# Kernel optimization log

Measured on AMD Instinct MI355X. Metric: run time of the kernel, lower is better.

## Reference

```python
import jax, jax.numpy as jnp
import numpy as np

GRID_D = 1024
SEQ_D = 1024
POS_D = 512
H = 16
HEAD = SEQ_D // H
MULT = 4
EPS = 1e-5


def layer_norm(x, g, b, eps=EPS):
    mu = jnp.mean(x, axis=-1, keepdims=True)
    var = jnp.mean(jnp.square(x - mu), axis=-1, keepdims=True)
    return (x - mu) * jax.lax.rsqrt(var + eps) * g + b


def setup_inputs() -> dict:
    key = jax.random.key(0)
    ks = jax.random.split(key, 12)
    std = 0.02
    B, N, M, L = 16, 16, 16, 1024
    return {
        "grid": jax.random.normal(ks[0], (B, N, M, GRID_D), jnp.float32),
        "query_pos": jax.random.normal(ks[1], (B, L, POS_D), jnp.float32),
        "Wq": jax.random.normal(ks[2], (POS_D, SEQ_D), jnp.float32) * std,
        "Wk": jax.random.normal(ks[3], (GRID_D, SEQ_D), jnp.float32) * std,
        "Wv": jax.random.normal(ks[4], (GRID_D, SEQ_D), jnp.float32) * std,
        "Wo": jax.random.normal(ks[5], (SEQ_D, SEQ_D), jnp.float32) * std,
        "ln_grid_g": jnp.ones((SEQ_D,), jnp.float32),
        "ln_grid_b": jnp.zeros((SEQ_D,), jnp.float32),
        "ln_q_g": jnp.ones((POS_D,), jnp.float32),
        "ln_q_b": jnp.zeros((POS_D,), jnp.float32),
        "ln_mlp_g": jnp.ones((SEQ_D,), jnp.float32),
        "ln_mlp_b": jnp.zeros((SEQ_D,), jnp.float32),
        "W1": jax.random.normal(ks[6], (SEQ_D, MULT * SEQ_D), jnp.float32) * std,
        "b1": jnp.zeros((MULT * SEQ_D,), jnp.float32),
        "W2": jax.random.normal(ks[7], (MULT * SEQ_D, SEQ_D), jnp.float32) * std,
        "b2": jnp.zeros((SEQ_D,), jnp.float32),
    }


def reference(grid, query_pos, Wq, Wk, Wv, Wo,
              ln_grid_g, ln_grid_b, ln_q_g, ln_q_b, ln_mlp_g, ln_mlp_b,
              W1, b1, W2, b2):
    B, N, M, _ = grid.shape
    T = N * M
    grid_flat = grid.reshape(B, T, GRID_D)
    K = layer_norm(jnp.einsum('btd,de->bte', grid_flat, Wk), ln_grid_g, ln_grid_b)
    V = jnp.einsum('btd,de->bte', grid_flat, Wv)
    qn = layer_norm(query_pos, ln_q_g, ln_q_b)
    Q = jnp.einsum('bld,de->ble', qn, Wq)  # (B, L, seq_d)
    L = Q.shape[1]
    # split heads: (B, H, len, head)
    Qh = Q.reshape(B, L, H, HEAD).transpose(0, 2, 1, 3)
    Kh = K.reshape(B, T, H, HEAD).transpose(0, 2, 1, 3)
    Vh = V.reshape(B, T, H, HEAD).transpose(0, 2, 1, 3)
    scale = 1.0 / np.sqrt(HEAD).astype(np.float32)
    scores = jnp.einsum('bhld,bhmd->bhlm', Qh, Kh) * scale
    probs = jax.nn.softmax(scores, axis=-1)
    attn = jnp.einsum('bhlm,bhmd->bhld', probs, Vh)
    attn = attn.transpose(0, 2, 1, 3).reshape(B, L, SEQ_D)
    attn = jnp.einsum('bld,de->ble', attn, Wo)
    x = Q + attn  # Q_proj in the torch code equals Q
    xn = layer_norm(x, ln_mlp_g, ln_mlp_b)
    h = jax.nn.gelu(jnp.einsum('bld,dh->blh', xn, W1) + b1)
    mlp_out = jnp.einsum('blh,hd->bld', h, W2) + b2
    return x + mlp_out
```

## Files before the change

kernel.cpp:

```cpp
#include <hip/hip_runtime.h>
#include <hip/hip_bf16.h>
#include <stdint.h>

typedef unsigned short u16;
typedef __bf16 bf16x8 __attribute__((ext_vector_type(8)));
typedef float f32x4 __attribute__((ext_vector_type(4)));

__device__ __forceinline__ float bf2f(unsigned int u) {
  union { float f; unsigned int i; } v; v.i = u << 16; return v.f;
}
__device__ __forceinline__ u16 f2bf(float f) {
  union { float f; unsigned int i; } v; v.f = f;
  unsigned int r = v.i + 0x7fffu + ((v.i >> 16) & 1u);
  return (u16)(r >> 16);
}

__device__ __forceinline__ float fast_gelu(float u) {
  const float z = -u * (1.5957691216057308f + 0.07135481282121989f * u * u);
  return u * __builtin_amdgcn_rcpf(1.0f + __expf(z));
}

__device__ __forceinline__ void gl_lds16(const void* g, void* l) {
  __builtin_amdgcn_global_load_lds(
      (const __attribute__((address_space(1))) unsigned int*)(uintptr_t)g,
      (__attribute__((address_space(3))) unsigned int*)(uintptr_t)l,
      16, 0, 0);
}

__global__ __launch_bounds__(256) void k_cast_bf16(const float* __restrict__ in,
                                                   u16* __restrict__ out, int n4) {
  int i = blockIdx.x * blockDim.x + threadIdx.x;
  if (i < n4) {
    float4 v = ((const float4*)in)[i];
    ushort4 o;
    o.x = f2bf(v.x); o.y = f2bf(v.y); o.z = f2bf(v.z); o.w = f2bf(v.w);
    ((ushort4*)out)[i] = o;
  }
}

__global__ __launch_bounds__(256) void k_transpose_cast(const float* __restrict__ in,
                                                        u16* __restrict__ out,
                                                        int K, int N) {
  __shared__ float tile[64][65];
  const int k0 = blockIdx.y * 64, n0 = blockIdx.x * 64;
  const int t = threadIdx.x;
#pragma unroll
  for (int i = 0; i < 16; i++) {
    int lin = t + i * 256, kk = lin >> 6, nn = lin & 63;
    tile[kk][nn] = in[(size_t)(k0 + kk) * N + n0 + nn];
  }
  __syncthreads();
#pragma unroll
  for (int i = 0; i < 16; i++) {
    int lin = t + i * 256, nn = lin >> 6, kk = lin & 63;
    out[(size_t)(n0 + nn) * K + k0 + kk] = f2bf(tile[kk][nn]);
  }
}

__global__ __launch_bounds__(256) void k_transpose3(const float* __restrict__ in0,
                                                    const float* __restrict__ in1,
                                                    const float* __restrict__ in2,
                                                    u16* __restrict__ out0,
                                                    u16* __restrict__ out1,
                                                    u16* __restrict__ out2) {
  __shared__ float tile[64][65];
  const float* in = (blockIdx.z == 0) ? in0 : (blockIdx.z == 1) ? in1 : in2;
  u16* out = (blockIdx.z == 0) ? out0 : (blockIdx.z == 1) ? out1 : out2;
  const int k0 = blockIdx.y * 64, n0 = blockIdx.x * 64;
  const int t = threadIdx.x;
#pragma unroll
  for (int i = 0; i < 16; i++) {
    int lin = t + i * 256, kk = lin >> 6, nn = lin & 63;
    tile[kk][nn] = in[(size_t)(k0 + kk) * 1024 + n0 + nn];
  }
  __syncthreads();
#pragma unroll
  for (int i = 0; i < 16; i++) {
    int lin = t + i * 256, nn = lin >> 6, kk = lin & 63;
    out[(size_t)(n0 + nn) * 1024 + k0 + kk] = f2bf(tile[kk][nn]);
  }
}

template <int RL>
__global__ __launch_bounds__(256) void k_ln_f32(const float* __restrict__ in,
                                                u16* __restrict__ out,
                                                const float* __restrict__ g,
                                                const float* __restrict__ b, int nrows) {
  const int wid = threadIdx.x >> 6, lane = threadIdx.x & 63;
  const int row = blockIdx.x * 4 + wid;
  if (row >= nrows) return;
  constexpr int PER = RL / 64;
  constexpr int NC = PER / 4;
  const float* p = in + (size_t)row * RL;
  float v[PER];
#pragma unroll
  for (int i = 0; i < NC; i++) {
    float4 f = ((const float4*)p)[lane + i * 64];
    v[i * 4 + 0] = f.x; v[i * 4 + 1] = f.y; v[i * 4 + 2] = f.z; v[i * 4 + 3] = f.w;
  }
  float s = 0.f, ss = 0.f;
#pragma unroll
  for (int i = 0; i < PER; i++) { s += v[i]; ss += v[i] * v[i]; }
#pragma unroll
  for (int o = 32; o; o >>= 1) { s += __shfl_xor(s, o, 64); ss += __shfl_xor(ss, o, 64); }
  const float mu = s * (1.0f / RL);
  const float var = ss * (1.0f / RL) - mu * mu;
  const float rs = rsqrtf(var + 1e-5f);
  u16* op = out + (size_t)row * RL;
#pragma unroll
  for (int i = 0; i < NC; i++) {
    ushort4 o;
    int c = (lane + i * 64) * 4;
    o.x = f2bf((v[i * 4 + 0] - mu) * rs * g[c + 0] + b[c + 0]);
    o.y = f2bf((v[i * 4 + 1] - mu) * rs * g[c + 1] + b[c + 1]);
    o.z = f2bf((v[i * 4 + 2] - mu) * rs * g[c + 2] + b[c + 2]);
    o.w = f2bf((v[i * 4 + 3] - mu) * rs * g[c + 3] + b[c + 3]);
    ((ushort4*)op)[lane + i * 64] = o;
  }
}

__global__ __launch_bounds__(256) void k_ln_bf16(const u16* __restrict__ in,
                                                 u16* __restrict__ out,
                                                 const float* __restrict__ g,
                                                 const float* __restrict__ b, int nrows) {
  const int wid = threadIdx.x >> 6, lane = threadIdx.x & 63;
  const int row = blockIdx.x * 4 + wid;
  if (row >= nrows) return;
  const u16* p = in + (size_t)row * 1024;
  float v[16];
#pragma unroll
  for (int i = 0; i < 2; i++) {
    uint4 u = ((const uint4*)p)[lane + i * 64];
    unsigned int w[4] = {u.x, u.y, u.z, u.w};
#pragma unroll
    for (int q = 0; q < 4; q++) {
      v[i * 8 + q * 2 + 0] = bf2f(w[q] & 0xffffu);
      v[i * 8 + q * 2 + 1] = bf2f(w[q] >> 16);
    }
  }
  float s = 0.f, ss = 0.f;
#pragma unroll
  for (int i = 0; i < 16; i++) { s += v[i]; ss += v[i] * v[i]; }
#pragma unroll
  for (int o = 32; o; o >>= 1) { s += __shfl_xor(s, o, 64); ss += __shfl_xor(ss, o, 64); }
  const float mu = s * (1.0f / 1024.f);
  const float var = ss * (1.0f / 1024.f) - mu * mu;
  const float rs = rsqrtf(var + 1e-5f);
  u16* op = out + (size_t)row * 1024;
#pragma unroll
  for (int i = 0; i < 2; i++) {
    uint4 u;
    unsigned int w[4];
#pragma unroll
    for (int q = 0; q < 4; q++) {
      int c = (lane + i * 64) * 8 + q * 2;
      u16 lo = f2bf((v[i * 8 + q * 2 + 0] - mu) * rs * g[c + 0] + b[c + 0]);
      u16 hi = f2bf((v[i * 8 + q * 2 + 1] - mu) * rs * g[c + 1] + b[c + 1]);
      w[q] = (unsigned int)lo | ((unsigned int)hi << 16);
    }
    u.x = w[0]; u.y = w[1]; u.z = w[2]; u.w = w[3];
    ((uint4*)op)[lane + i * 64] = u;
  }
}

#define E_BF16 0
#define E_ADD_BF16 1
#define E_GELU_BF16 4
#define E_BIAS_RESB_OUT 5
#define E_KV 6
#define E_ACC 7

template <int BM, int BN, int WR, int WC, int EPI>
__global__ __launch_bounds__(256) void k_gemm_bt(
    const u16* __restrict__ A, const u16* __restrict__ B,
    int K, int lda, int ldb, int ldc,
    void* C0, void* C1) {
  constexpr int AM = BM / WR / 16;
  constexpr int AN = BN / WC / 16;
  constexpr int ACH = BM / 8;
  constexpr int NCH = (BM + BN) / 8;

  __shared__ u16 As[BM * 64];
  __shared__ u16 Bs[BN * 64];

  const int tid = threadIdx.x;
  const int lane = tid & 63;
  const int wid = tid >> 6;
  const int wr = wid / WC;
  const int wc = wid % WC;

  const int bm = blockIdx.y * BM;
  const int bn = blockIdx.x * BN;

  const u16* Ab = A + (size_t)bm * lda;
  const u16* Bb = B + (size_t)bn * ldb;

  const int r8 = lane >> 3;
  const int c8e = (lane & 7) * 8;

  f32x4 acc[AM][AN];
  const f32x4 vzero = {0.f, 0.f, 0.f, 0.f};
#pragma unroll
  for (int m = 0; m < AM; m++)
#pragma unroll
    for (int n = 0; n < AN; n++) acc[m][n] = vzero;

  const int NK = K / 64;
  for (int kt = 0; kt < NK; kt++) {
    const int k0 = kt * 64;
#pragma unroll
    for (int i = 0; i < NCH / 4; i++) {
      const int ch = wid + i * 4;
      if (ch < ACH) {
        gl_lds16(Ab + (size_t)(ch * 8 + r8) * lda + k0 + c8e, As + ch * 512);
      } else {
        const int c2 = ch - ACH;
        gl_lds16(Bb + (size_t)(c2 * 8 + r8) * ldb + k0 + c8e, Bs + c2 * 512);
      }
    }
    __syncthreads();
#pragma unroll
    for (int kk = 0; kk < 2; kk++) {
      bf16x8 af[AM], bfr[AN];
#pragma unroll
      for (int m = 0; m < AM; m++)
        af[m] = *(const bf16x8*)&As[(wr * (BM / WR) + m * 16 + (lane & 15)) * 64 +
                                    kk * 32 + (lane >> 4) * 8];
#pragma unroll
      for (int n = 0; n < AN; n++)
        bfr[n] = *(const bf16x8*)&Bs[(wc * (BN / WC) + n * 16 + (lane & 15)) * 64 +
                                     kk * 32 + (lane >> 4) * 8];
#pragma unroll
      for (int m = 0; m < AM; m++)
#pragma unroll
        for (int n = 0; n < AN; n++)
          acc[m][n] = __builtin_amdgcn_mfma_f32_16x16x32_bf16(af[m], bfr[n], acc[m][n], 0, 0, 0);
    }
    if (kt + 1 < NK) __syncthreads();
  }

  const int lr = (lane >> 4) * 4;
  const int lc = lane & 15;
#pragma unroll
  for (int m = 0; m < AM; m++) {
    const int gr0 = bm + wr * (BM / WR) + m * 16 + lr;
#pragma unroll
    for (int n = 0; n < AN; n++) {
      const int gc = bn + wc * (BN / WC) + n * 16 + lc;
#pragma unroll
      for (int j = 0; j < 4; j++) {
        const int gr = gr0 + j;
        const float v = acc[m][n][j];
        if constexpr (EPI == E_KV) {
          if (gc < 1024) {
            ((u16*)C0)[(size_t)gr * 1024 + gc] = f2bf(v);
          } else {
            const int b_ = gr >> 8, t_ = gr & 255, g2 = gc - 1024, h_ = g2 >> 6, d_ = g2 & 63;
            ((u16*)C1)[(((size_t)(b_ * 16 + h_) * 64 + d_) << 8) + t_] = f2bf(v);
          }
        } else {
          ((u16*)C0)[(size_t)gr * ldc + gc] = f2bf(v);
        }
      }
    }
  }
}

template <int EPI>
__global__ __launch_bounds__(512, 2) void k_gemm2(
    const u16* __restrict__ A, const u16* __restrict__ B,
    int K, int lda, int ldb, int ldc,
    void* C0, void* C1, const float* __restrict__ bias) {
  __shared__ u16 smem[2][2][256 * 64];

  const int tid = threadIdx.x;
  const int lane = tid & 63;
  const int wid = tid >> 6;
  const int wr = wid >> 2;
  const int wc = wid & 3;

  const int nwg = gridDim.x * gridDim.y;
  const int lid = blockIdx.y * gridDim.x + blockIdx.x;
  const int q = nwg >> 3, r = nwg & 7;
  const int xcd = lid & 7, loc = lid >> 3;
  const int id = (xcd < r ? xcd * (q + 1) : r * (q + 1) + (xcd - r) * q) + loc;
  const int bm = (id / gridDim.x) * 256;
  const int bn = (id % gridDim.x) * 256;

  const u16* Ab = A + (size_t)bm * lda;
  const u16* Bb = B + (size_t)bn * ldb;

  const int r8 = lane >> 3;
  const int ceSw = (((lane & 7) ^ r8) << 3);

  f32x4 acc[8][4];
  const f32x4 vzero = {0.f, 0.f, 0.f, 0.f};
#pragma unroll
  for (int m = 0; m < 8; m++)
#pragma unroll
    for (int n = 0; n < 4; n++) acc[m][n] = vzero;

  const int NK = K / 64;

  auto stage = [&](int bi, int kt) {
    const int k0 = kt * 64;
    u16* As = &smem[bi][0][0];
    u16* Bs = &smem[bi][1][0];
#pragma unroll
    for (int i = 0; i < 4; i++) {
      const int c = wid * 4 + i;
      gl_lds16(Ab + (size_t)(c * 8 + r8) * lda + k0 + ceSw, As + c * 512);
    }
#pragma unroll
    for (int i = 0; i < 4; i++) {
      const int c = wid * 4 + i;
      gl_lds16(Bb + (size_t)(c * 8 + r8) * ldb + k0 + ceSw, Bs + c * 512);
    }
  };

  stage(0, 0);
  __syncthreads();

  int cur = 0;
  for (int kt = 0; kt < NK; kt++) {
    if (kt + 1 < NK) stage(cur ^ 1, kt + 1);
    const u16* As = &smem[cur][0][0];
    const u16* Bs = &smem[cur][1][0];
#pragma unroll
    for (int kk = 0; kk < 2; kk++) {
      const int csw = (kk * 32 + (lane >> 4) * 8) ^ ((lane & 7) << 3);
      bf16x8 af[8], bfv[4];
#pragma unroll
      for (int m = 0; m < 8; m++)
        af[m] = *(const bf16x8*)&As[(wr * 128 + m * 16 + (lane & 15)) * 64 + csw];
#pragma unroll
      for (int n = 0; n < 4; n++)
        bfv[n] = *(const bf16x8*)&Bs[(wc * 64 + n * 16 + (lane & 15)) * 64 + csw];
#pragma unroll
      for (int m = 0; m < 8; m++)
#pragma unroll
        for (int n = 0; n < 4; n++)
          acc[m][n] = __builtin_amdgcn_mfma_f32_16x16x32_bf16(af[m], bfv[n], acc[m][n], 0, 0, 0);
    }
    __syncthreads();
    cur ^= 1;
  }

  const int lr = (lane >> 4) * 4;
  const int lc = lane & 15;
#pragma unroll
  for (int m = 0; m < 8; m++) {
    const int gr0 = bm + wr * 128 + m * 16 + lr;
#pragma unroll
    for (int n = 0; n < 4; n++) {
      const int gc = bn + wc * 64 + n * 16 + lc;
#pragma unroll
      for (int j = 0; j < 4; j++) {
        const int gr = gr0 + j;
        const float v = acc[m][n][j];
        const size_t ci = (size_t)gr * ldc + gc;
        if constexpr (EPI == E_BF16) {
          ((u16*)C0)[ci] = f2bf(v);
        } else if constexpr (EPI == E_ADD_BF16) {
          ((u16*)C0)[ci] = f2bf(v + bf2f(((const u16*)C1)[ci]));
        } else if constexpr (EPI == E_GELU_BF16) {
          ((u16*)C0)[ci] = f2bf(fast_gelu(v + bias[gc]));
        } else if constexpr (EPI == E_BIAS_RESB_OUT) {
          ((float*)C0)[ci] = v + bias[gc] + bf2f(((const u16*)C1)[ci]);
        } else if constexpr (EPI == E_ACC) {
          ((float*)C0)[ci] += v;
        }
      }
    }
  }
}

__global__ __launch_bounds__(256) void k_attn(const u16* __restrict__ qb,
                                              const u16* __restrict__ kb,
                                              const u16* __restrict__ vt,
                                              u16* __restrict__ ob) {
  __shared__ u16 plds[4][32][264];
  const int lane = threadIdx.x & 63, wid = threadIdx.x >> 6;
  const int lc = lane & 15, g = lane >> 4;
  const int qt = blockIdx.x;
  const int bh = blockIdx.y;
  const int b = bh >> 4, h = bh & 15;

  const u16* qp = qb + (((size_t)b * 1024 + qt * 128 + wid * 32) << 10) + h * 64;
  const u16* kp = kb + (((size_t)b * 256) << 10) + h * 64;
  const u16* vp = vt + (((size_t)(b * 16 + h)) << 14);

  f32x4 acc[2][16];
  const f32x4 vzero = {0.f, 0.f, 0.f, 0.f};
#pragma unroll
  for (int m = 0; m < 2; m++)
#pragma unroll
    for (int n = 0; n < 16; n++) acc[m][n] = vzero;

  bf16x8 af[2][2];
#pragma unroll
  for (int m = 0; m < 2; m++)
#pragma unroll
    for (int kk = 0; kk < 2; kk++)
      af[m][kk] = *(const bf16x8*)(qp + ((size_t)(m * 16 + lc) << 10) + kk * 32 + g * 8);

#pragma unroll
  for (int n = 0; n < 16; n++) {
#pragma unroll
    for (int kk = 0; kk < 2; kk++) {
      bf16x8 bv = *(const bf16x8*)(kp + ((size_t)(n * 16 + lc) << 10) + kk * 32 + g * 8);
#pragma unroll
      for (int m = 0; m < 2; m++)
        acc[m][n] = __builtin_amdgcn_mfma_f32_16x16x32_bf16(af[m][kk], bv, acc[m][n], 0, 0, 0);
    }
  }

  const float sc = 0.125f;
#pragma unroll
  for (int m = 0; m < 2; m++) {
#pragma unroll
    for (int j = 0; j < 4; j++) {
      float mx = acc[m][0][j];
#pragma unroll
      for (int n = 1; n < 16; n++) mx = fmaxf(mx, acc[m][n][j]);
#pragma unroll
      for (int o = 1; o < 16; o <<= 1) mx = fmaxf(mx, __shfl_xor(mx, o, 64));
      mx *= sc;
      float sm = 0.f;
#pragma unroll
      for (int n = 0; n < 16; n++) {
        float p = __expf(sc * acc[m][n][j] - mx);
        acc[m][n][j] = p;
        sm += p;
      }
#pragma unroll
      for (int o = 1; o < 16; o <<= 1) sm += __shfl_xor(sm, o, 64);
      const float inv = 1.0f / sm;
      const int rowl = m * 16 + g * 4 + j;
#pragma unroll
      for (int n = 0; n < 16; n++)
        plds[wid][rowl][n * 16 + lc] = f2bf(acc[m][n][j] * inv);
    }
  }

  f32x4 acc2[2][4];
#pragma unroll
  for (int m = 0; m < 2; m++)
#pragma unroll
    for (int n = 0; n < 4; n++) acc2[m][n] = vzero;

#pragma unroll
  for (int kt = 0; kt < 8; kt++) {
    bf16x8 pa[2];
#pragma unroll
    for (int m = 0; m < 2; m++)
      pa[m] = *(const bf16x8*)&plds[wid][m * 16 + lc][kt * 32 + g * 8];
#pragma unroll
    for (int n = 0; n < 4; n++) {
      bf16x8 vv = *(const bf16x8*)(vp + (size_t)(n * 16 + lc) * 256 + kt * 32 + g * 8);
#pragma unroll
      for (int m = 0; m < 2; m++)
        acc2[m][n] = __builtin_amdgcn_mfma_f32_16x16x32_bf16(pa[m], vv, acc2[m][n], 0, 0, 0);
    }
  }

#pragma unroll
  for (int m = 0; m < 2; m++) {
#pragma unroll
    for (int n = 0; n < 4; n++) {
#pragma unroll
      for (int j = 0; j < 4; j++) {
        const int gr = qt * 128 + wid * 32 + m * 16 + g * 4 + j;
        const int gc = h * 64 + n * 16 + lc;
        ob[(((size_t)b * 1024 + gr) << 10) + gc] = f2bf(acc2[m][n][j]);
      }
    }
  }
}

extern "C" void kernel_launch(void* const* d_in, const int* in_sizes, int n_in,
                              void* d_out, int out_size, void* d_ws, size_t ws_size,
                              hipStream_t stream) {
  (void)in_sizes; (void)n_in; (void)out_size;
  const float* grid     = (const float*)d_in[0];
  const float* qpos     = (const float*)d_in[1];
  const float* Wq       = (const float*)d_in[2];
  const float* Wk       = (const float*)d_in[3];
  const float* Wv       = (const float*)d_in[4];
  const float* Wo       = (const float*)d_in[5];
  const float* ln_g_g   = (const float*)d_in[6];
  const float* ln_g_b   = (const float*)d_in[7];
  const float* ln_q_g   = (const float*)d_in[8];
  const float* ln_q_b   = (const float*)d_in[9];
  const float* ln_m_g   = (const float*)d_in[10];
  const float* ln_m_b   = (const float*)d_in[11];
  const float* W1       = (const float*)d_in[12];
  const float* b1       = (const float*)d_in[13];
  const float* W2       = (const float*)d_in[14];
  const float* b2       = (const float*)d_in[15];
  float* out = (float*)d_out;

  char* ws = (char*)d_ws;
  size_t off = 0;
  auto nxt = [&](size_t bytes) { size_t o = off; off += (bytes + 255) & ~(size_t)255; return o; };
  u16* wk_t  = (u16*)(ws + nxt(1024ull * 1024 * 2));
  u16* wv_t  = (u16*)(ws + nxt(1024ull * 1024 * 2));
  u16* wq_t  = (u16*)(ws + nxt(1024ull * 512 * 2));
  u16* wo_t  = (u16*)(ws + nxt(1024ull * 1024 * 2));
  u16* w1_t  = (u16*)(ws + nxt(4096ull * 1024 * 2));
  u16* w2_t  = (u16*)(ws + nxt(1024ull * 4096 * 2));
  u16* qslot = (u16*)(ws + nxt(16ull * 1024 * 1024 * 2));
  u16* xb    = (u16*)(ws + nxt(16ull * 1024 * 1024 * 2));
  const size_t regionOff = off;
  u16* gridb = (u16*)(ws + nxt(16ull * 256 * 1024 * 2));
  u16* qn    = (u16*)(ws + nxt(16ull * 1024 * 512 * 2));
  u16* kb    = (u16*)(ws + nxt(16ull * 256 * 1024 * 2));
  u16* vt    = (u16*)(ws + nxt(16ull * 16 * 64 * 256 * 2));
  u16* hbuf  = (u16*)(ws + regionOff);

  const int HC = (ws_size >= regionOff + (16384ull * 4096 * 2) + (1u << 20)) ? 4096 : 2048;

  u16* qb    = qslot;
  u16* x     = qslot;
  u16* attnb = xb;
  u16* xn    = xb;

  k_cast_bf16<<<4096, 256, 0, stream>>>(grid, gridb, 1048576);
  k_transpose3<<<dim3(16, 16, 3), 256, 0, stream>>>(Wk, Wv, Wo, wk_t, wv_t, wo_t);
  k_transpose_cast<<<dim3(16, 8), 256, 0, stream>>>(Wq, wq_t, 512, 1024);
  k_transpose_cast<<<dim3(64, 16), 256, 0, stream>>>(W1, w1_t, 1024, 4096);
  k_transpose_cast<<<dim3(16, 64), 256, 0, stream>>>(W2, w2_t, 4096, 1024);
  k_ln_f32<512><<<4096, 256, 0, stream>>>(qpos, qn, ln_q_g, ln_q_b, 16384);
  k_gemm_bt<128, 128, 2, 2, E_KV><<<dim3(16, 32), 256, 0, stream>>>(
      gridb, wk_t, 1024, 1024, 1024, 2048, kb, vt);
  k_ln_bf16<<<1024, 256, 0, stream>>>(kb, kb, ln_g_g, ln_g_b, 4096);
  k_gemm2<E_BF16><<<dim3(4, 64), 512, 0, stream>>>(
      qn, wq_t, 512, 512, 512, 1024, qb, nullptr, nullptr);
  k_attn<<<dim3(8, 256), 256, 0, stream>>>(qb, kb, vt, attnb);
  k_gemm2<E_ADD_BF16><<<dim3(4, 64), 512, 0, stream>>>(
      attnb, wo_t, 1024, 1024, 1024, 1024, x, qb, nullptr);
  k_ln_bf16<<<4096, 256, 0, stream>>>(x, xn, ln_m_g, ln_m_b, 16384);
  for (int c = 0; c < 4096 / HC; c++) {
    k_gemm2<E_GELU_BF16><<<dim3(HC / 256, 64), 512, 0, stream>>>(
        xn, w1_t + (size_t)c * HC * 1024, 1024, 1024, 1024, HC,
        hbuf, nullptr, b1 + c * HC);
    if (c == 0) {
      k_gemm2<E_BIAS_RESB_OUT><<<dim3(4, 64), 512, 0, stream>>>(
          hbuf, w2_t + c * HC, HC, HC, 4096, 1024, out, x, b2);
    } else {
      k_gemm2<E_ACC><<<dim3(4, 64), 512, 0, stream>>>(
          hbuf, w2_t + c * HC, HC, HC, 4096, 1024, out, nullptr, nullptr);
    }
  }
}
```

Before: 529.0 us.

## Route KV projection through pipelined 256x256 GEMM and regroup tiles per XCD

Drops the simple 128x128 single-buffered GEMM used for the fused K/V projection and runs it through the double-buffered 256x256 k_gemm2 kernel, adding a KV epilogue that writes K row-major and V transposed per head. It also changes the tile-to-XCD mapping when the workgroup count divides evenly, so each XCD processes groups of four adjacent column tiles over a contiguous run of rows, for better L2 reuse. The KV GEMM now launches only 128 workgroups, which may leave part of the GPU idle. The remapping also applies to the other GEMM launches.

```diff
diff --git a/kernel.cpp b/kernel.cpp
--- a/kernel.cpp
+++ b/kernel.cpp
@@ -170,102 +170,6 @@
 #define E_KV 6
 #define E_ACC 7
 
-template <int BM, int BN, int WR, int WC, int EPI>
-__global__ __launch_bounds__(256) void k_gemm_bt(
-    const u16* __restrict__ A, const u16* __restrict__ B,
-    int K, int lda, int ldb, int ldc,
-    void* C0, void* C1) {
-  constexpr int AM = BM / WR / 16;
-  constexpr int AN = BN / WC / 16;
-  constexpr int ACH = BM / 8;
-  constexpr int NCH = (BM + BN) / 8;
-
-  __shared__ u16 As[BM * 64];
-  __shared__ u16 Bs[BN * 64];
-
-  const int tid = threadIdx.x;
-  const int lane = tid & 63;
-  const int wid = tid >> 6;
-  const int wr = wid / WC;
-  const int wc = wid % WC;
-
-  const int bm = blockIdx.y * BM;
-  const int bn = blockIdx.x * BN;
-
-  const u16* Ab = A + (size_t)bm * lda;
-  const u16* Bb = B + (size_t)bn * ldb;
-
-  const int r8 = lane >> 3;
-  const int c8e = (lane & 7) * 8;
-
-  f32x4 acc[AM][AN];
-  const f32x4 vzero = {0.f, 0.f, 0.f, 0.f};
-#pragma unroll
-  for (int m = 0; m < AM; m++)
-#pragma unroll
-    for (int n = 0; n < AN; n++) acc[m][n] = vzero;
-
-  const int NK = K / 64;
-  for (int kt = 0; kt < NK; kt++) {
-    const int k0 = kt * 64;
-#pragma unroll
-    for (int i = 0; i < NCH / 4; i++) {
-      const int ch = wid + i * 4;
-      if (ch < ACH) {
-        gl_lds16(Ab + (size_t)(ch * 8 + r8) * lda + k0 + c8e, As + ch * 512);
-      } else {
-        const int c2 = ch - ACH;
-        gl_lds16(Bb + (size_t)(c2 * 8 + r8) * ldb + k0 + c8e, Bs + c2 * 512);
-      }
-    }
-    __syncthreads();
-#pragma unroll
-    for (int kk = 0; kk < 2; kk++) {
-      bf16x8 af[AM], bfr[AN];
-#pragma unroll
-      for (int m = 0; m < AM; m++)
-        af[m] = *(const bf16x8*)&As[(wr * (BM / WR) + m * 16 + (lane & 15)) * 64 +
-                                    kk * 32 + (lane >> 4) * 8];
-#pragma unroll
-      for (int n = 0; n < AN; n++)
-        bfr[n] = *(const bf16x8*)&Bs[(wc * (BN / WC) + n * 16 + (lane & 15)) * 64 +
-                                     kk * 32 + (lane >> 4) * 8];
-#pragma unroll
-      for (int m = 0; m < AM; m++)
-#pragma unroll
-        for (int n = 0; n < AN; n++)
-          acc[m][n] = __builtin_amdgcn_mfma_f32_16x16x32_bf16(af[m], bfr[n], acc[m][n], 0, 0, 0);
-    }
-    if (kt + 1 < NK) __syncthreads();
-  }
-
-  const int lr = (lane >> 4) * 4;
-  const int lc = lane & 15;
-#pragma unroll
-  for (int m = 0; m < AM; m++) {
-    const int gr0 = bm + wr * (BM / WR) + m * 16 + lr;
-#pragma unroll
-    for (int n = 0; n < AN; n++) {
-      const int gc = bn + wc * (BN / WC) + n * 16 + lc;
-#pragma unroll
-      for (int j = 0; j < 4; j++) {
-        const int gr = gr0 + j;
-        const float v = acc[m][n][j];
-        if constexpr (EPI == E_KV) {
-          if (gc < 1024) {
-            ((u16*)C0)[(size_t)gr * 1024 + gc] = f2bf(v);
-          } else {
-            const int b_ = gr >> 8, t_ = gr & 255, g2 = gc - 1024, h_ = g2 >> 6, d_ = g2 & 63;
-            ((u16*)C1)[(((size_t)(b_ * 16 + h_) * 64 + d_) << 8) + t_] = f2bf(v);
-          }
-        } else {
-          ((u16*)C0)[(size_t)gr * ldc + gc] = f2bf(v);
-        }
-      }
-    }
-  }
-}
-
 template <int EPI>
 __global__ __launch_bounds__(512, 2) void k_gemm2(
     const u16* __restrict__ A, const u16* __restrict__ B,
@@ -283,9 +187,19 @@
   const int lid = blockIdx.y * gridDim.x + blockIdx.x;
   const int q = nwg >> 3, r = nwg & 7;
   const int xcd = lid & 7, loc = lid >> 3;
-  const int id = (xcd < r ? xcd * (q + 1) : r * (q + 1) + (xcd - r) * q) + loc;
-  const int bm = (id / gridDim.x) * 256;
-  const int bn = (id % gridDim.x) * 256;
+  int bm, bn;
+  if (r == 0 && (q % gridDim.x) == 0 && (gridDim.x & 3) == 0) {
+    const int rpc = q / gridDim.x;
+    const int row0 = (xcd * q) / gridDim.x;
+    const int grpSz = rpc * 4;
+    const int grp = loc / grpSz, li = loc % grpSz;
+    bm = (row0 + li / 4) * 256;
+    bn = (grp * 4 + (li & 3)) * 256;
+  } else {
+    const int id = (xcd < r ? xcd * (q + 1) : r * (q + 1) + (xcd - r) * q) + loc;
+    bm = (id / gridDim.x) * 256;
+    bn = (id % gridDim.x) * 256;
+  }
 
   const u16* Ab = A + (size_t)bm * lda;
   const u16* Bb = B + (size_t)bn * ldb;
@@ -369,6 +283,13 @@
           ((float*)C0)[ci] = v + bias[gc] + bf2f(((const u16*)C1)[ci]);
         } else if constexpr (EPI == E_ACC) {
           ((float*)C0)[ci] += v;
+        } else if constexpr (EPI == E_KV) {
+          if (gc < 1024) {
+            ((u16*)C0)[(size_t)gr * 1024 + gc] = f2bf(v);
+          } else {
+            const int b_ = gr >> 8, t_ = gr & 255, g2 = gc - 1024, h_ = g2 >> 6, d_ = g2 & 63;
+            ((u16*)C1)[(((size_t)(b_ * 16 + h_) * 64 + d_) << 8) + t_] = f2bf(v);
+          }
         }
       }
     }
@@ -531,8 +452,8 @@
   k_transpose_cast<<<dim3(64, 16), 256, 0, stream>>>(W1, w1_t, 1024, 4096);
   k_transpose_cast<<<dim3(16, 64), 256, 0, stream>>>(W2, w2_t, 4096, 1024);
   k_ln_f32<512><<<4096, 256, 0, stream>>>(qpos, qn, ln_q_g, ln_q_b, 16384);
-  k_gemm_bt<128, 128, 2, 2, E_KV><<<dim3(16, 32), 256, 0, stream>>>(
-      gridb, wk_t, 1024, 1024, 1024, 2048, kb, vt);
+  k_gemm2<E_KV><<<dim3(8, 16), 512, 0, stream>>>(
+      gridb, wk_t, 1024, 1024, 1024, 2048, kb, vt, nullptr);
   k_ln_bf16<<<1024, 256, 0, stream>>>(kb, kb, ln_g_g, ln_g_b, 4096);
   k_gemm2<E_BF16><<<dim3(4, 64), 512, 0, stream>>>(
       qn, wq_t, 512, 512, 512, 1024, qb, nullptr, nullptr);
```

Result: no change. 537.5 us (+1.6%).

## Merge prep kernels into one launch and fuse KV and Q GEMMs

Applied to the files above, without the earlier changes.

Collapses the grid cast, all weight transposes and the query LayerNorm into a single block-indexed prep kernel. It also replaces the separate KV GEMM and Q GEMM with one 256x256-tile kernel that uses double-buffered, XOR-swizzled LDS staging and dispatches blocks to either problem. The aim is to cut launch overhead and tail idle time, and to improve GEMM efficiency through larger tiles and load overlap. The cost is a more complex branchy kernel, and 384 large blocks of uneven K length may load-balance poorly.

```diff
diff --git a/kernel.cpp b/kernel.cpp
--- a/kernel.cpp
+++ b/kernel.cpp
@@ -27,23 +27,75 @@
       16, 0, 0);
 }
 
-__global__ __launch_bounds__(256) void k_cast_bf16(const float* __restrict__ in,
-                                                   u16* __restrict__ out, int n4) {
-  int i = blockIdx.x * blockDim.x + threadIdx.x;
-  if (i < n4) {
-    float4 v = ((const float4*)in)[i];
+__global__ __launch_bounds__(256) void k_prep(
+    const float* __restrict__ grid, u16* __restrict__ gridb,
+    const float* __restrict__ Wk, u16* __restrict__ wk_t,
+    const float* __restrict__ Wv, u16* __restrict__ wv_t,
+    const float* __restrict__ Wo, u16* __restrict__ wo_t,
+    const float* __restrict__ Wq, u16* __restrict__ wq_t,
+    const float* __restrict__ W1, u16* __restrict__ w1_t,
+    const float* __restrict__ W2, u16* __restrict__ w2_t,
+    const float* __restrict__ qpos, u16* __restrict__ qn,
+    const float* __restrict__ g512, const float* __restrict__ b512) {
+  __shared__ float tile[64][65];
+  const int b = blockIdx.x, t = threadIdx.x;
+
+  if (b < 4096) {
+    const int i = b * 256 + t;
+    float4 v = ((const float4*)grid)[i];
     ushort4 o;
     o.x = f2bf(v.x); o.y = f2bf(v.y); o.z = f2bf(v.z); o.w = f2bf(v.w);
-    ((ushort4*)out)[i] = o;
-  }
-}
-
-__global__ __launch_bounds__(256) void k_transpose_cast(const float* __restrict__ in,
-                                                        u16* __restrict__ out,
-                                                        int K, int N) {
-  __shared__ float tile[64][65];
-  const int k0 = blockIdx.y * 64, n0 = blockIdx.x * 64;
-  const int t = threadIdx.x;
+    ((ushort4*)gridb)[i] = o;
+    return;
+  }
+  if (b >= 7040) {
+    const int wid = t >> 6, lane = t & 63;
+    const int row = (b - 7040) * 4 + wid;
+    const float* p = qpos + (size_t)row * 512;
+    float v[8];
+#pragma unroll
+    for (int i = 0; i < 2; i++) {
+      float4 f = ((const float4*)p)[lane + i * 64];
+      v[i * 4 + 0] = f.x; v[i * 4 + 1] = f.y; v[i * 4 + 2] = f.z; v[i * 4 + 3] = f.w;
+    }
+    float s = 0.f, ss = 0.f;
+#pragma unroll
+    for (int i = 0; i < 8; i++) { s += v[i]; ss += v[i] * v[i]; }
+#pragma unroll
+    for (int o = 32; o; o >>= 1) { s += __shfl_xor(s, o, 64); ss += __shfl_xor(ss, o, 64); }
+    const float mu = s * (1.0f / 512.f);
+    const float var = ss * (1.0f / 512.f) - mu * mu;
+    const float rs = rsqrtf(var + 1e-5f);
+    u16* op = qn + (size_t)row * 512;
+#pragma unroll
+    for (int i = 0; i < 2; i++) {
+      ushort4 o;
+      int c = (lane + i * 64) * 4;
+      o.x = f2bf((v[i * 4 + 0] - mu) * rs * g512[c + 0] + b512[c + 0]);
+      o.y = f2bf((v[i * 4 + 1] - mu) * rs * g512[c + 1] + b512[c + 1]);
+      o.z = f2bf((v[i * 4 + 2] - mu) * rs * g512[c + 2] + b512[c + 2]);
+      o.w = f2bf((v[i * 4 + 3] - mu) * rs * g512[c + 3] + b512[c + 3]);
+      ((ushort4*)op)[lane + i * 64] = o;
+    }
+    return;
+  }
+  const float* in; u16* out; int K, N, bx, by;
+  if (b < 4864) {
+    const int t3 = b - 4096, z = t3 >> 8, r = t3 & 255;
+    bx = r & 15; by = r >> 4; K = 1024; N = 1024;
+    in = (z == 0) ? Wk : (z == 1) ? Wv : Wo;
+    out = (z == 0) ? wk_t : (z == 1) ? wv_t : wo_t;
+  } else if (b < 4992) {
+    const int t4 = b - 4864;
+    bx = t4 & 15; by = t4 >> 4; K = 512; N = 1024; in = Wq; out = wq_t;
+  } else if (b < 6016) {
+    const int t5 = b - 4992;
+    bx = t5 % 64; by = t5 / 64; K = 1024; N = 4096; in = W1; out = w1_t;
+  } else {
+    const int t6 = b - 6016;
+    bx = t6 & 15; by = t6 >> 4; K = 4096; N = 1024; in = W2; out = w2_t;
+  }
+  const int k0 = by * 64, n0 = bx * 64;
 #pragma unroll
   for (int i = 0; i < 16; i++) {
     int lin = t + i * 256, kk = lin >> 6, nn = lin & 63;
@@ -54,68 +106,6 @@
   for (int i = 0; i < 16; i++) {
     int lin = t + i * 256, nn = lin >> 6, kk = lin & 63;
     out[(size_t)(n0 + nn) * K + k0 + kk] = f2bf(tile[kk][nn]);
-  }
-}
-
-__global__ __launch_bounds__(256) void k_transpose3(const float* __restrict__ in0,
-                                                    const float* __restrict__ in1,
-                                                    const float* __restrict__ in2,
-                                                    u16* __restrict__ out0,
-                                                    u16* __restrict__ out1,
-                                                    u16* __restrict__ out2) {
-  __shared__ float tile[64][65];
-  const float* in = (blockIdx.z == 0) ? in0 : (blockIdx.z == 1) ? in1 : in2;
-  u16* out = (blockIdx.z == 0) ? out0 : (blockIdx.z == 1) ? out1 : out2;
-  const int k0 = blockIdx.y * 64, n0 = blockIdx.x * 64;
-  const int t = threadIdx.x;
-#pragma unroll
-  for (int i = 0; i < 16; i++) {
-    int lin = t + i * 256, kk = lin >> 6, nn = lin & 63;
-    tile[kk][nn] = in[(size_t)(k0 + kk) * 1024 + n0 + nn];
-  }
-  __syncthreads();
-#pragma unroll
-  for (int i = 0; i < 16; i++) {
-    int lin = t + i * 256, nn = lin >> 6, kk = lin & 63;
-    out[(size_t)(n0 + nn) * 1024 + k0 + kk] = f2bf(tile[kk][nn]);
-  }
-}
-
-template <int RL>
-__global__ __launch_bounds__(256) void k_ln_f32(const float* __restrict__ in,
-                                                u16* __restrict__ out,
-                                                const float* __restrict__ g,
-                                                const float* __restrict__ b, int nrows) {
-  const int wid = threadIdx.x >> 6, lane = threadIdx.x & 63;
-  const int row = blockIdx.x * 4 + wid;
-  if (row >= nrows) return;
-  constexpr int PER = RL / 64;
-  constexpr int NC = PER / 4;
-  const float* p = in + (size_t)row * RL;
-  float v[PER];
-#pragma unroll
-  for (int i = 0; i < NC; i++) {
-    float4 f = ((const float4*)p)[lane + i * 64];
-    v[i * 4 + 0] = f.x; v[i * 4 + 1] = f.y; v[i * 4 + 2] = f.z; v[i * 4 + 3] = f.w;
-  }
-  float s = 0.f, ss = 0.f;
-#pragma unroll
-  for (int i = 0; i < PER; i++) { s += v[i]; ss += v[i] * v[i]; }
-#pragma unroll
-  for (int o = 32; o; o >>= 1) { s += __shfl_xor(s, o, 64); ss += __shfl_xor(ss, o, 64); }
-  const float mu = s * (1.0f / RL);
-  const float var = ss * (1.0f / RL) - mu * mu;
-  const float rs = rsqrtf(var + 1e-5f);
-  u16* op = out + (size_t)row * RL;
-#pragma unroll
-  for (int i = 0; i < NC; i++) {
-    ushort4 o;
-    int c = (lane + i * 64) * 4;
-    o.x = f2bf((v[i * 4 + 0] - mu) * rs * g[c + 0] + b[c + 0]);
-    o.y = f2bf((v[i * 4 + 1] - mu) * rs * g[c + 1] + b[c + 1]);
-    o.z = f2bf((v[i * 4 + 2] - mu) * rs * g[c + 2] + b[c + 2]);
-    o.w = f2bf((v[i * 4 + 3] - mu) * rs * g[c + 3] + b[c + 3]);
-    ((ushort4*)op)[lane + i * 64] = o;
   }
 }
 
@@ -167,104 +157,7 @@
 #define E_ADD_BF16 1
 #define E_GELU_BF16 4
 #define E_BIAS_RESB_OUT 5
-#define E_KV 6
 #define E_ACC 7
-
-template <int BM, int BN, int WR, int WC, int EPI>
-__global__ __launch_bounds__(256) void k_gemm_bt(
-    const u16* __restrict__ A, const u16* __restrict__ B,
-    int K, int lda, int ldb, int ldc,
-    void* C0, void* C1) {
-  constexpr int AM = BM / WR / 16;
-  constexpr int AN = BN / WC / 16;
-  constexpr int ACH = BM / 8;
-  constexpr int NCH = (BM + BN) / 8;
-
-  __shared__ u16 As[BM * 64];
-  __shared__ u16 Bs[BN * 64];
-
-  const int tid = threadIdx.x;
-  const int lane = tid & 63;
-  const int wid = tid >> 6;
-  const int wr = wid / WC;
-  const int wc = wid % WC;
-
-  const int bm = blockIdx.y * BM;
-  const int bn = blockIdx.x * BN;
-
-  const u16* Ab = A + (size_t)bm * lda;
-  const u16* Bb = B + (size_t)bn * ldb;
-
-  const int r8 = lane >> 3;
-  const int c8e = (lane & 7) * 8;
-
-  f32x4 acc[AM][AN];
-  const f32x4 vzero = {0.f, 0.f, 0.f, 0.f};
-#pragma unroll
-  for (int m = 0; m < AM; m++)
-#pragma unroll
-    for (int n = 0; n < AN; n++) acc[m][n] = vzero;
-
-  const int NK = K / 64;
-  for (int kt = 0; kt < NK; kt++) {
-    const int k0 = kt * 64;
-#pragma unroll
-    for (int i = 0; i < NCH / 4; i++) {
-      const int ch = wid + i * 4;
-      if (ch < ACH) {
-        gl_lds16(Ab + (size_t)(ch * 8 + r8) * lda + k0 + c8e, As + ch * 512);
-      } else {
-        const int c2 = ch - ACH;
-        gl_lds16(Bb + (size_t)(c2 * 8 + r8) * ldb + k0 + c8e, Bs + c2 * 512);
-      }
-    }
-    __syncthreads();
-#pragma unroll
-    for (int kk = 0; kk < 2; kk++) {
-      bf16x8 af[AM], bfr[AN];
-#pragma unroll
-      for (int m = 0; m < AM; m++)
-        af[m] = *(const bf16x8*)&As[(wr * (BM / WR) + m * 16 + (lane & 15)) * 64 +
-                                    kk * 32 + (lane >> 4) * 8];
-#pragma unroll
-      for (int n = 0; n < AN; n++)
-        bfr[n] = *(const bf16x8*)&Bs[(wc * (BN / WC) + n * 16 + (lane & 15)) * 64 +
-                                     kk * 32 + (lane >> 4) * 8];
-#pragma unroll
-      for (int m = 0; m < AM; m++)
-#pragma unroll
-        for (int n = 0; n < AN; n++)
-          acc[m][n] = __builtin_amdgcn_mfma_f32_16x16x32_bf16(af[m], bfr[n], acc[m][n], 0, 0, 0);
-    }
-    if (kt + 1 < NK) __syncthreads();
-  }
-
-  const int lr = (lane >> 4) * 4;
-  const int lc = lane & 15;
-#pragma unroll
-  for (int m = 0; m < AM; m++) {
-    const int gr0 = bm + wr * (BM / WR) + m * 16 + lr;
-#pragma unroll
-    for (int n = 0; n < AN; n++) {
-      const int gc = bn + wc * (BN / WC) + n * 16 + lc;
-#pragma unroll
-      for (int j = 0; j < 4; j++) {
-        const int gr = gr0 + j;
-        const float v = acc[m][n][j];
-        if constexpr (EPI == E_KV) {
-          if (gc < 1024) {
-            ((u16*)C0)[(size_t)gr * 1024 + gc] = f2bf(v);
-          } else {
-            const int b_ = gr >> 8, t_ = gr & 255, g2 = gc - 1024, h_ = g2 >> 6, d_ = g2 & 63;
-            ((u16*)C1)[(((size_t)(b_ * 16 + h_) * 64 + d_) << 8) + t_] = f2bf(v);
-          }
-        } else {
-          ((u16*)C0)[(size_t)gr * ldc + gc] = f2bf(v);
-        }
-      }
-    }
-  }
-}
 
 template <int EPI>
 __global__ __launch_bounds__(512, 2) void k_gemm2(
@@ -369,6 +262,118 @@
           ((float*)C0)[ci] = v + bias[gc] + bf2f(((const u16*)C1)[ci]);
         } else if constexpr (EPI == E_ACC) {
           ((float*)C0)[ci] += v;
+        }
+      }
+    }
+  }
+}
+
+__global__ __launch_bounds__(512, 2) void k_gemm_qkv(
+    const u16* __restrict__ gridb, const u16* __restrict__ wkv,
+    const u16* __restrict__ qn, const u16* __restrict__ wq,
+    u16* __restrict__ kb, u16* __restrict__ vt, u16* __restrict__ qb) {
+  __shared__ u16 smem[2][2][256 * 64];
+
+  const int tid = threadIdx.x;
+  const int lane = tid & 63;
+  const int wid = tid >> 6;
+  const int wr = wid >> 2;
+  const int wc = wid & 3;
+
+  const int bid = blockIdx.x;
+  const bool isKV = (bid < 128);
+  const u16* A; const u16* B;
+  int K, lda, bm, bn;
+  if (isKV) {
+    A = gridb; B = wkv; K = 1024; lda = 1024;
+    bm = (bid >> 3) * 256; bn = (bid & 7) * 256;
+  } else {
+    const int id = bid - 128;
+    A = qn; B = wq; K = 512; lda = 512;
+    bm = (id >> 2) * 256; bn = (id & 3) * 256;
+  }
+  const int ldb = lda;
+
+  const u16* Ab = A + (size_t)bm * lda;
+  const u16* Bb = B + (size_t)bn * ldb;
+
+  const int r8 = lane >> 3;
+  const int ceSw = (((lane & 7) ^ r8) << 3);
+
+  f32x4 acc[8][4];
+  const f32x4 vzero = {0.f, 0.f, 0.f, 0.f};
+#pragma unroll
+  for (int m = 0; m < 8; m++)
+#pragma unroll
+    for (int n = 0; n < 4; n++) acc[m][n] = vzero;
+
+  const int NK = K / 64;
+
+  auto stage = [&](int bi, int kt) {
+    const int k0 = kt * 64;
+    u16* As = &smem[bi][0][0];
+    u16* Bs = &smem[bi][1][0];
+#pragma unroll
+    for (int i = 0; i < 4; i++) {
+      const int c = wid * 4 + i;
+      gl_lds16(Ab + (size_t)(c * 8 + r8) * lda + k0 + ceSw, As + c * 512);
+    }
+#pragma unroll
+    for (int i = 0; i < 4; i++) {
+      const int c = wid * 4 + i;
+      gl_lds16(Bb + (size_t)(c * 8 + r8) * ldb + k0 + ceSw, Bs + c * 512);
+    }
+  };
+
+  stage(0, 0);
+  __syncthreads();
+
+  int cur = 0;
+  for (int kt = 0; kt < NK; kt++) {
+    if (kt + 1 < NK) stage(cur ^ 1, kt + 1);
+    const u16* As = &smem[cur][0][0];
+    const u16* Bs = &smem[cur][1][0];
+#pragma unroll
+    for (int kk = 0; kk < 2; kk++) {
+      const int csw = (kk * 32 + (lane >> 4) * 8) ^ ((lane & 7) << 3);
+      bf16x8 af[8], bfv[4];
+#pragma unroll
+      for (int m = 0; m < 8; m++)
+        af[m] = *(const bf16x8*)&As[(wr * 128 + m * 16 + (lane & 15)) * 64 + csw];
+#pragma unroll
+      for (int n = 0; n < 4; n++)
+        bfv[n] = *(const bf16x8*)&Bs[(wc * 64 + n * 16 + (lane & 15)) * 64 + csw];
+#pragma unroll
+      for (int m = 0; m < 8; m++)
+#pragma unroll
+        for (int n = 0; n < 4; n++)
+          acc[m][n] = __builtin_amdgcn_mfma_f32_16x16x32_bf16(af[m], bfv[n], acc[m][n], 0, 0, 0);
+    }
+    __syncthreads();
+    cur ^= 1;
+  }
+
+  const int lr = (lane >> 4) * 4;
+  const int lc = lane & 15;
+#pragma unroll
+  for (int m = 0; m < 8; m++) {
+    const int gr0 = bm + wr * 128 + m * 16 + lr;
+#pragma unroll
+    for (int n = 0; n < 4; n++) {
+      const int gc = bn + wc * 64 + n * 16 + lc;
+#pragma unroll
+      for (int j = 0; j < 4; j++) {
+        const int gr = gr0 + j;
+        const float v = acc[m][n][j];
+        if (isKV) {
+          if (gc < 1024) {
+            kb[(size_t)gr * 1024 + gc] = f2bf(v);
+          } else {
+            const int b_ = gr >> 8, t_ = gr & 255, g2 = gc - 1024, h_ = g2 >> 6, d_ = g2 & 63;
+            vt[(((size_t)(b_ * 16 + h_) * 64 + d_) << 8) + t_] = f2bf(v);
+          }
+        } else {
+          qb[(size_t)gr * 1024 + gc] = f2bf(v);
         }
       }
     }
@@ -525,17 +530,11 @@
   u16* attnb = xb;
   u16* xn    = xb;
 
-  k_cast_bf16<<<4096, 256, 0, stream>>>(grid, gridb, 1048576);
-  k_transpose3<<<dim3(16, 16, 3), 256, 0, stream>>>(Wk, Wv, Wo, wk_t, wv_t, wo_t);
-  k_transpose_cast<<<dim3(16, 8), 256, 0, stream>>>(Wq, wq_t, 512, 1024);
-  k_transpose_cast<<<dim3(64, 16), 256, 0, stream>>>(W1, w1_t, 1024, 4096);
-  k_transpose_cast<<<dim3(16, 64), 256, 0, stream>>>(W2, w2_t, 4096, 1024);
-  k_ln_f32<512><<<4096, 256, 0, stream>>>(qpos, qn, ln_q_g, ln_q_b, 16384);
-  k_gemm_bt<128, 128, 2, 2, E_KV><<<dim3(16, 32), 256, 0, stream>>>(
-      gridb, wk_t, 1024, 1024, 1024, 2048, kb, vt);
+  k_prep<<<11136, 256, 0, stream>>>(grid, gridb, Wk, wk_t, Wv, wv_t, Wo, wo_t,
+                                    Wq, wq_t, W1, w1_t, W2, w2_t,
+                                    qpos, qn, ln_q_g, ln_q_b);
+  k_gemm_qkv<<<384, 512, 0, stream>>>(gridb, wk_t, qn, wq_t, kb, vt, qb);
   k_ln_bf16<<<1024, 256, 0, stream>>>(kb, kb, ln_g_g, ln_g_b, 4096);
-  k_gemm2<E_BF16><<<dim3(4, 64), 512, 0, stream>>>(
-      qn, wq_t, 512, 512, 512, 1024, qb, nullptr, nullptr);
   k_attn<<<dim3(8, 256), 256, 0, stream>>>(qb, kb, vt, attnb);
   k_gemm2<E_ADD_BF16><<<dim3(4, 64), 512, 0, stream>>>(
       attnb, wo_t, 1024, 1024, 1024, 1024, x, qb, nullptr);
```

After: 518.4 us (median of 2 runs). -2.0%, faster.
